# Kernel tuning notes

Hardware: AMD Instinct MI355X
Metric: run time of the kernel (lower is better)

Reference implementation:

```python
import jax, jax.numpy as jnp
import numpy as np

F0_DIM, PH_DIM, MIDI_DIM, DUR_DIM = 64, 128, 64, 64
COND = 256
TOTAL = F0_DIM + PH_DIM + MIDI_DIM + DUR_DIM  # 320
EPS = 1e-5


def setup_inputs() -> dict:
    key = jax.random.key(0)
    ks = jax.random.split(key, 16)
    B, T = 16, 4096
    inp = {
        "f0": jax.random.uniform(ks[0], (B, T), jnp.float32) * 400.0 + 80.0,
        "phone": jax.random.randint(ks[1], (B, T), 0, 100, jnp.int32),
        "duration": jax.random.uniform(ks[2], (B, T), jnp.float32),
        "midi": jax.random.randint(ks[3], (B, T), 0, 128, jnp.int32),
        # f0 encoder: Linear(1,32) -> ReLU -> Linear(32,64)
        "f0_w1": jax.random.normal(ks[4], (1, F0_DIM // 2), jnp.float32) * 0.1,
        "f0_b1": jnp.zeros((F0_DIM // 2,), jnp.float32),
        "f0_w2": jax.random.normal(ks[5], (F0_DIM // 2, F0_DIM), jnp.float32) * 0.1,
        "f0_b2": jnp.zeros((F0_DIM,), jnp.float32),
        # embeddings
        "phone_table": jax.random.normal(ks[6], (100, PH_DIM), jnp.float32),
        "midi_table": jax.random.normal(ks[7], (128, MIDI_DIM), jnp.float32),
        # duration encoder: Linear(1,32) -> ReLU -> Linear(32,64)
        "dur_w1": jax.random.normal(ks[8], (1, DUR_DIM // 2), jnp.float32) * 0.1,
        "dur_b1": jnp.zeros((DUR_DIM // 2,), jnp.float32),
        "dur_w2": jax.random.normal(ks[9], (DUR_DIM // 2, DUR_DIM), jnp.float32) * 0.1,
        "dur_b2": jnp.zeros((DUR_DIM,), jnp.float32),
        # projection: Linear(320,256) -> LayerNorm(256) -> ReLU -> Linear(256,256)
        "proj_w1": jax.random.normal(ks[10], (TOTAL, COND), jnp.float32) * (1.0 / np.sqrt(TOTAL)),
        "proj_b1": jnp.zeros((COND,), jnp.float32),
        "ln_g": jnp.ones((COND,), jnp.float32),
        "ln_b": jnp.zeros((COND,), jnp.float32),
        "proj_w2": jax.random.normal(ks[11], (COND, COND), jnp.float32) * (1.0 / np.sqrt(COND)),
        "proj_b2": jnp.zeros((COND,), jnp.float32),
    }
    return inp


def reference(f0, phone, duration, midi,
              f0_w1, f0_b1, f0_w2, f0_b2,
              phone_table, midi_table,
              dur_w1, dur_b1, dur_w2, dur_b2,
              proj_w1, proj_b1, ln_g, ln_b, proj_w2, proj_b2):
    # f0 / duration MLPs, vectorized over all (batch, time) positions
    f0_h = jax.nn.relu(f0[..., None] * f0_w1[0] + f0_b1)            # [B,T,32]
    f0_emb = f0_h @ f0_w2 + f0_b2                                    # [B,T,64]
    dur_h = jax.nn.relu(duration[..., None] * dur_w1[0] + dur_b1)    # [B,T,32]
    dur_emb = dur_h @ dur_w2 + dur_b2                                # [B,T,64]
    phone_emb = phone_table[phone]                                   # [B,T,128]
    midi_emb = midi_table[midi]                                      # [B,T,64]
    combined = jnp.concatenate([f0_emb, phone_emb, midi_emb, dur_emb], axis=-1)  # [B,T,320]
    h = combined @ proj_w1 + proj_b1                                 # [B,T,256]
    mu = jnp.mean(h, axis=-1, keepdims=True)
    var = jnp.mean((h - mu) ** 2, axis=-1, keepdims=True)
    h = (h - mu) * jax.lax.rsqrt(var + EPS) * ln_g + ln_b
    h = jax.nn.relu(h)
    return h @ proj_w2 + proj_b2                                     # [B,T,256]
```

## Files before the change

### kernel.cpp

```cpp
#include <hip/hip_runtime.h>

typedef _Float16 f16x8 __attribute__((ext_vector_type(8)));
typedef float f32x4 __attribute__((ext_vector_type(4)));
typedef unsigned int u32x2 __attribute__((ext_vector_type(2)));

#define MROWS 65536
#define BM 64
#define NBLK (MROWS / BM)

#define B1F_OFF 0u
#define B2F_OFF 65536u
#define TP_OFF 196608u
#define TM_OFF 299008u
#define BC_OFF 430080u
#define WFD_OFF 431104u


__device__ __forceinline__ unsigned afoff(unsigned X) {
  return (X * 16u) ^ ((X & 0x38u) << 1);
}

__global__ __launch_bounds__(256) void prep_tables(
    const float* __restrict__ f0_w2, const float* __restrict__ f0_b2,
    const float* __restrict__ ptab, const float* __restrict__ mtab,
    const float* __restrict__ dur_w2, const float* __restrict__ dur_b2,
    const float* __restrict__ W1, const float* __restrict__ pb1,
    float* __restrict__ wsf) {
  const int r = blockIdx.x, n = threadIdx.x;
  if (r < 64) {
    float s = 0.f;
    if (r < 32) {
      for (int j = 0; j < 64; ++j) s = fmaf(f0_w2[r * 64 + j], W1[j * 256 + n], s);
    } else {
      for (int j = 0; j < 64; ++j) s = fmaf(dur_w2[(r - 32) * 64 + j], W1[(256 + j) * 256 + n], s);
    }
    wsf[WFD_OFF / 4 + r * 256 + n] = s;
  } else if (r < 164) {
    const int p = r - 64;
    float s = 0.f;
    for (int j = 0; j < 128; ++j) s = fmaf(ptab[p * 128 + j], W1[(64 + j) * 256 + n], s);
    wsf[TP_OFF / 4 + p * 256 + n] = s;
  } else if (r < 292) {
    const int m = r - 164;
    float s = 0.f;
    for (int j = 0; j < 64; ++j) s = fmaf(mtab[m * 64 + j], W1[(192 + j) * 256 + n], s);
    wsf[TM_OFF / 4 + m * 256 + n] = s;
  } else {
    float s = pb1[n];
    for (int j = 0; j < 64; ++j) {
      s = fmaf(f0_b2[j], W1[j * 256 + n], s);
      s = fmaf(dur_b2[j], W1[(256 + j) * 256 + n], s);
    }
    wsf[BC_OFF / 4 + n] = s;
  }
}

__global__ __launch_bounds__(64) void prep_frags(const float* __restrict__ W2, char* __restrict__ ws) {
  const float* Wfd = (const float*)(ws + WFD_OFF);
  const int t = blockIdx.x;
  const int l = threadIdx.x;
  const int qq = l >> 4, c = l & 15;
  if (t < 64) {
    const int kt = t >> 4, nt = t & 15;
    const int col = (nt >> 2) * 64 + c * 4 + (nt & 3);
    f16x8 v;
#pragma unroll
    for (int e = 0; e < 8; ++e) {
      const int k = kt * 32 + 4 * qq + (e & 3) + 16 * (e >> 2);
      v[e] = (_Float16)Wfd[(k & 63) * 256 + col];
    }
    *(f16x8*)(ws + B1F_OFF + (unsigned)((kt * 16 + nt) * 64 + l) * 16u) = v;
  } else {
    const int t2 = t - 64;
    const int kt = t2 >> 4, nt = t2 & 15;
    const int col = (nt >> 2) * 64 + c * 4 + (nt & 3);
    f16x8 v;
#pragma unroll
    for (int e = 0; e < 8; ++e) {
      const int k = kt * 32 + 4 * qq + (e & 3) + 16 * (e >> 2);
      v[e] = (_Float16)W2[k * 256 + col];
    }
    *(f16x8*)(ws + B2F_OFF + (unsigned)((kt * 16 + nt) * 64 + l) * 16u) = v;
  }
}

__global__ __launch_bounds__(256, 2) void cond_enc_main(
    const float* __restrict__ f0g, const int* __restrict__ phone,
    const float* __restrict__ durg, const int* __restrict__ midi,
    const float* __restrict__ f0_w1, const float* __restrict__ f0_b1,
    const float* __restrict__ dur_w1, const float* __restrict__ dur_b1,
    const float* __restrict__ ln_g, const float* __restrict__ ln_b,
    const float* __restrict__ pb2, const char* __restrict__ ws,
    float* __restrict__ out) {
  __shared__ __align__(16) unsigned char smem[32768 + 3072];
  unsigned char* Afrag = smem;
  float* partials = (float*)(smem + 32768);

  const int tid = threadIdx.x;
  const int l = tid & 63;
  const int wc = tid >> 6;
  const int q = l >> 4;
  const int c = l & 15;
  const int b = blockIdx.x;

  const float* Tp = (const float*)(ws + TP_OFF);
  const float* Tm = (const float*)(ws + TM_OFF);

  const float xf_all = f0g[b * BM + l];
  const float xd_all = durg[b * BM + l];
  const int ph_all = phone[b * BM + l];
  const int md_all = midi[b * BM + l];

  const f32x4 zero4 = {0.f, 0.f, 0.f, 0.f};
  f32x4 acc[4][4];
#pragma unroll
  for (int i = 0; i < 4; ++i)
#pragma unroll
    for (int j = 0; j < 4; ++j) acc[i][j] = zero4;
  {
    const f16x8* B1p = (const f16x8*)(ws + B1F_OFF);
#pragma unroll
    for (int h = 0; h < 2; ++h) {
      f16x8 a1[2][4];
#pragma unroll
      for (int ii = 0; ii < 2; ++ii) {
        const int i = h * 2 + ii;
        const float xf = __shfl(xf_all, i * 16 + c);
        const float xd = __shfl(xd_all, i * 16 + c);
#pragma unroll
        for (int kh = 0; kh < 2; ++kh) {
          f16x8 hi, lo;
#pragma unroll
          for (int e = 0; e < 8; ++e) {
            const int ki = 4 * q + (e & 3) + 16 * (e >> 2);
            const float wv = kh ? dur_w1[ki] : f0_w1[ki];
            const float bv = kh ? dur_b1[ki] : f0_b1[ki];
            const float x = kh ? xd : xf;
            const float a = fmaxf(fmaf(x, wv, bv), 0.f);
            const _Float16 hh = (_Float16)a;
            hi[e] = hh;
            lo[e] = (_Float16)(a - (float)hh);
          }
          a1[ii][kh] = hi;
          a1[ii][kh + 2] = lo;
        }
      }
#pragma unroll
      for (int kt = 0; kt < 4; ++kt) {
        f16x8 b4[4];
#pragma unroll
        for (int j = 0; j < 4; ++j) b4[j] = B1p[(kt * 16 + wc * 4 + j) * 64 + l];
#pragma unroll
        for (int ii = 0; ii < 2; ++ii)
#pragma unroll
          for (int j = 0; j < 4; ++j)
            acc[h * 2 + ii][j] =
                __builtin_amdgcn_mfma_f32_16x16x32_f16(a1[ii][kt], b4[j], acc[h * 2 + ii][j], 0, 0, 0);
      }
    }
  }

  const f32x4 bc4 = *(const f32x4*)((const float*)(ws + BC_OFF) + wc * 64 + c * 4);
  float psum[4][4], psq[4][4];
#pragma unroll
  for (int i = 0; i < 4; ++i) {
#pragma unroll
    for (int r = 0; r < 4; ++r) {
      const int ph = __shfl(ph_all, i * 16 + q * 4 + r);
      const int md = __shfl(md_all, i * 16 + q * 4 + r);
      const f32x4 tp4 = *(const f32x4*)(Tp + ph * 256 + wc * 64 + c * 4);
      const f32x4 tm4 = *(const f32x4*)(Tm + md * 256 + wc * 64 + c * 4);
      float s = 0.f, ss = 0.f;
#pragma unroll
      for (int j = 0; j < 4; ++j) {
        float v = acc[i][j][r] + bc4[j] + tp4[j] + tm4[j];
        acc[i][j][r] = v;
        s += v;
        ss = fmaf(v, v, ss);
      }
      psum[i][r] = s;
      psq[i][r] = ss;
    }
  }
#pragma unroll
  for (int i = 0; i < 4; ++i)
#pragma unroll
    for (int r = 0; r < 4; ++r) {
      float s = psum[i][r], ss = psq[i][r];
#pragma unroll
      for (int m = 1; m < 16; m <<= 1) {
        s += __shfl_xor(s, m, 64);
        ss += __shfl_xor(ss, m, 64);
      }
      psum[i][r] = s;
      psq[i][r] = ss;
    }
  if (c == 0) {
#pragma unroll
    for (int i = 0; i < 4; ++i)
#pragma unroll
      for (int r = 0; r < 4; ++r) {
        const int row = i * 16 + q * 4 + r;
        partials[row * 12 + wc * 2 + 0] = psum[i][r];
        partials[row * 12 + wc * 2 + 1] = psq[i][r];
      }
  }
  __syncthreads();

  const f32x4 g4 = *(const f32x4*)(ln_g + wc * 64 + c * 4);
  const f32x4 lb4 = *(const f32x4*)(ln_b + wc * 64 + c * 4);
  const int kt_pk = wc * 2 + (c >> 3);
  const int lp_base = 16 * (c & 3);
  const unsigned hoff = (unsigned)((c >> 2) & 1) * 8u;
#pragma unroll
  for (int i = 0; i < 4; ++i) {
#pragma unroll
    for (int r = 0; r < 4; ++r) {
      const int row = i * 16 + q * 4 + r;
      const f32x4 pa = *(const f32x4*)(partials + row * 12);
      const f32x4 pb = *(const f32x4*)(partials + row * 12 + 4);
      const float s = pa[0] + pa[2] + pb[0] + pb[2];
      const float ss = pa[1] + pa[3] + pb[1] + pb[3];
      const float mu = s * (1.f / 256.f);
      const float var = fmaxf(ss * (1.f / 256.f) - mu * mu, 0.f);
      const float rstd = rsqrtf(var + 1e-5f);
      unsigned short hw[4];
#pragma unroll
      for (int j = 0; j < 4; ++j) {
        float v = fmaf((acc[i][j][r] - mu) * rstd, g4[j], lb4[j]);
        v = fmaxf(v, 0.f);
        hw[j] = __builtin_bit_cast(unsigned short, (_Float16)v);
      }
      u32x2 pkt;
      pkt[0] = (unsigned)hw[0] | ((unsigned)hw[1] << 16);
      pkt[1] = (unsigned)hw[2] | ((unsigned)hw[3] << 16);
      const unsigned X = (unsigned)((kt_pk * 4 + i) * 64 + (q * 4 + r + lp_base));
      *(u32x2*)(Afrag + afoff(X) + hoff) = pkt;
    }
  }
  __syncthreads();

#pragma unroll
  for (int i = 0; i < 4; ++i)
#pragma unroll
    for (int j = 0; j < 4; ++j) acc[i][j] = zero4;
  {
    const f16x8* B2p = (const f16x8*)(ws + B2F_OFF);
#pragma unroll
    for (int kt = 0; kt < 8; ++kt) {
      f16x8 a4[4], b4[4];
#pragma unroll
      for (int i = 0; i < 4; ++i)
        a4[i] = *(const f16x8*)(Afrag + afoff((unsigned)((kt * 4 + i) * 64 + l)));
#pragma unroll
      for (int j = 0; j < 4; ++j) b4[j] = B2p[(kt * 16 + wc * 4 + j) * 64 + l];
#pragma unroll
      for (int i = 0; i < 4; ++i)
#pragma unroll
        for (int j = 0; j < 4; ++j)
          acc[i][j] = __builtin_amdgcn_mfma_f32_16x16x32_f16(a4[i], b4[j], acc[i][j], 0, 0, 0);
    }
  }
  const f32x4 b24 = *(const f32x4*)(pb2 + wc * 64 + c * 4);
#pragma unroll
  for (int i = 0; i < 4; ++i)
#pragma unroll
    for (int r = 0; r < 4; ++r) {
      const int grow = b * BM + i * 16 + q * 4 + r;
      f32x4 st;
#pragma unroll
      for (int j = 0; j < 4; ++j) st[j] = acc[i][j][r] + b24[j];
      __builtin_nontemporal_store(st, (f32x4*)(out + grow * 256 + wc * 64 + c * 4));
    }
}

extern "C" void kernel_launch(void* const* d_in, const int* in_sizes, int n_in,
                              void* d_out, int out_size, void* d_ws, size_t ws_size,
                              hipStream_t stream) {
  (void)in_sizes; (void)n_in; (void)out_size; (void)ws_size;
  const float* f0 = (const float*)d_in[0];
  const int* phone = (const int*)d_in[1];
  const float* dur = (const float*)d_in[2];
  const int* midi = (const int*)d_in[3];
  const float* f0_w1 = (const float*)d_in[4];
  const float* f0_b1 = (const float*)d_in[5];
  const float* f0_w2 = (const float*)d_in[6];
  const float* f0_b2 = (const float*)d_in[7];
  const float* ptab = (const float*)d_in[8];
  const float* mtab = (const float*)d_in[9];
  const float* dur_w1 = (const float*)d_in[10];
  const float* dur_b1 = (const float*)d_in[11];
  const float* dur_w2 = (const float*)d_in[12];
  const float* dur_b2 = (const float*)d_in[13];
  const float* W1 = (const float*)d_in[14];
  const float* pb1 = (const float*)d_in[15];
  const float* ln_g = (const float*)d_in[16];
  const float* ln_b = (const float*)d_in[17];
  const float* W2 = (const float*)d_in[18];
  const float* pb2 = (const float*)d_in[19];
  char* ws = (char*)d_ws;
  float* out = (float*)d_out;

  prep_tables<<<293, 256, 0, stream>>>(f0_w2, f0_b2, ptab, mtab, dur_w2, dur_b2, W1, pb1, (float*)ws);
  prep_frags<<<192, 64, 0, stream>>>(W2, ws);
  cond_enc_main<<<NBLK, 256, 0, stream>>>(f0, phone, dur, midi, f0_w1, f0_b1, dur_w1, dur_b1,
                                          ln_g, ln_b, pb2, ws, out);
}
```

Baseline: 42.30 us.

## Split fused encoder into two kernels via fp16 fragment buffer; drop hi/lo split

The fused kernel is split into two kernels when the workspace is large enough. Stage 1 computes the first projection plus LayerNorm and ReLU, then writes fp16 MFMA-ready A fragments to a 32 MB workspace buffer. Stage 2 runs the second GEMM with 512-thread blocks and no LDS staging. Separately, the first GEMM's hi/lo fp16 split of the f0/duration hidden activations is removed, halving its K and MFMA count at the cost of precision. The split adds a global round trip for the intermediate but may improve occupancy and reduce LDS pressure.

```diff
diff --git a/kernel.cpp b/kernel.cpp
--- a/kernel.cpp
+++ b/kernel.cpp
@@ -5,8 +5,6 @@
 typedef unsigned int u32x2 __attribute__((ext_vector_type(2)));
 
 #define MROWS 65536
-#define BM 64
-#define NBLK (MROWS / BM)
 
 #define B1F_OFF 0u
 #define B2F_OFF 65536u
@@ -14,6 +12,8 @@
 #define TM_OFF 299008u
 #define BC_OFF 430080u
 #define WFD_OFF 431104u
+#define HFRAG_OFF 524288u
+#define WS_NEED (524288u + 33554432u)
 
 
 __device__ __forceinline__ unsigned afoff(unsigned X) {
@@ -60,18 +60,18 @@
   const int t = blockIdx.x;
   const int l = threadIdx.x;
   const int qq = l >> 4, c = l & 15;
-  if (t < 64) {
+  if (t < 32) {
     const int kt = t >> 4, nt = t & 15;
     const int col = (nt >> 2) * 64 + c * 4 + (nt & 3);
     f16x8 v;
 #pragma unroll
     for (int e = 0; e < 8; ++e) {
       const int k = kt * 32 + 4 * qq + (e & 3) + 16 * (e >> 2);
-      v[e] = (_Float16)Wfd[(k & 63) * 256 + col];
+      v[e] = (_Float16)Wfd[k * 256 + col];
     }
     *(f16x8*)(ws + B1F_OFF + (unsigned)((kt * 16 + nt) * 64 + l) * 16u) = v;
   } else {
-    const int t2 = t - 64;
+    const int t2 = t - 32;
     const int kt = t2 >> 4, nt = t2 & 15;
     const int col = (nt >> 2) * 64 + c * 4 + (nt & 3);
     f16x8 v;
@@ -84,7 +84,208 @@
   }
 }
 
-__global__ __launch_bounds__(256, 2) void cond_enc_main(
+__global__ __launch_bounds__(256, 2) void enc_stage1(
+    const float* __restrict__ f0g, const int* __restrict__ phone,
+    const float* __restrict__ durg, const int* __restrict__ midi,
+    const float* __restrict__ f0_w1, const float* __restrict__ f0_b1,
+    const float* __restrict__ dur_w1, const float* __restrict__ dur_b1,
+    const float* __restrict__ ln_g, const float* __restrict__ ln_b,
+    const char* __restrict__ ws, char* __restrict__ hfrag) {
+  __shared__ __align__(16) float partials[64 * 12];
+
+  const int tid = threadIdx.x;
+  const int l = tid & 63;
+  const int wc = tid >> 6;
+  const int q = l >> 4;
+  const int c = l & 15;
+  const int b = blockIdx.x;
+
+  const float* Tp = (const float*)(ws + TP_OFF);
+  const float* Tm = (const float*)(ws + TM_OFF);
+
+  const float xf_all = f0g[b * 64 + l];
+  const float xd_all = durg[b * 64 + l];
+  const int ph_all = phone[b * 64 + l];
+  const int md_all = midi[b * 64 + l];
+
+  f16x8 a1[4][2];
+#pragma unroll
+  for (int i = 0; i < 4; ++i) {
+    const float xf = __shfl(xf_all, i * 16 + c);
+    const float xd = __shfl(xd_all, i * 16 + c);
+#pragma unroll
+    for (int kh = 0; kh < 2; ++kh) {
+      f16x8 v;
+#pragma unroll
+      for (int e = 0; e < 8; ++e) {
+        const int ki = 4 * q + (e & 3) + 16 * (e >> 2);
+        const float wv = kh ? dur_w1[ki] : f0_w1[ki];
+        const float bv = kh ? dur_b1[ki] : f0_b1[ki];
+        const float x = kh ? xd : xf;
+        v[e] = (_Float16)fmaxf(fmaf(x, wv, bv), 0.f);
+      }
+      a1[i][kh] = v;
+    }
+  }
+
+  const f32x4 zero4 = {0.f, 0.f, 0.f, 0.f};
+  f32x4 acc[4][4];
+#pragma unroll
+  for (int i = 0; i < 4; ++i)
+#pragma unroll
+    for (int j = 0; j < 4; ++j) acc[i][j] = zero4;
+  {
+    const f16x8* B1p = (const f16x8*)(ws + B1F_OFF);
+#pragma unroll
+    for (int kt = 0; kt < 2; ++kt) {
+      f16x8 b4[4];
+#pragma unroll
+      for (int j = 0; j < 4; ++j) b4[j] = B1p[(kt * 16 + wc * 4 + j) * 64 + l];
+#pragma unroll
+      for (int i = 0; i < 4; ++i)
+#pragma unroll
+        for (int j = 0; j < 4; ++j)
+          acc[i][j] = __builtin_amdgcn_mfma_f32_16x16x32_f16(a1[i][kt], b4[j], acc[i][j], 0, 0, 0);
+    }
+  }
+
+  const f32x4 bc4 = *(const f32x4*)((const float*)(ws + BC_OFF) + wc * 64 + c * 4);
+  float psum[4][4], psq[4][4];
+#pragma unroll
+  for (int i = 0; i < 4; ++i) {
+#pragma unroll
+    for (int r = 0; r < 4; ++r) {
+      const int ph = __shfl(ph_all, i * 16 + q * 4 + r);
+      const int md = __shfl(md_all, i * 16 + q * 4 + r);
+      const f32x4 tp4 = *(const f32x4*)(Tp + ph * 256 + wc * 64 + c * 4);
+      const f32x4 tm4 = *(const f32x4*)(Tm + md * 256 + wc * 64 + c * 4);
+      float s = 0.f, ss = 0.f;
+#pragma unroll
+      for (int j = 0; j < 4; ++j) {
+        float v = acc[i][j][r] + bc4[j] + tp4[j] + tm4[j];
+        acc[i][j][r] = v;
+        s += v;
+        ss = fmaf(v, v, ss);
+      }
+      psum[i][r] = s;
+      psq[i][r] = ss;
+    }
+  }
+#pragma unroll
+  for (int i = 0; i < 4; ++i)
+#pragma unroll
+    for (int r = 0; r < 4; ++r) {
+      float s = psum[i][r], ss = psq[i][r];
+#pragma unroll
+      for (int m = 1; m < 16; m <<= 1) {
+        s += __shfl_xor(s, m, 64);
+        ss += __shfl_xor(ss, m, 64);
+      }
+      psum[i][r] = s;
+      psq[i][r] = ss;
+    }
+  if (c == 0) {
+#pragma unroll
+    for (int i = 0; i < 4; ++i)
+#pragma unroll
+      for (int r = 0; r < 4; ++r) {
+        const int row = i * 16 + q * 4 + r;
+        partials[row * 12 + wc * 2 + 0] = psum[i][r];
+        partials[row * 12 + wc * 2 + 1] = psq[i][r];
+      }
+  }
+  __syncthreads();
+
+  float mu_r, rs_r;
+  {
+    const f32x4 pa = *(const f32x4*)(partials + l * 12);
+    const f32x4 pb = *(const f32x4*)(partials + l * 12 + 4);
+    const float s = pa[0] + pa[2] + pb[0] + pb[2];
+    const float ss = pa[1] + pa[3] + pb[1] + pb[3];
+    mu_r = s * (1.f / 256.f);
+    const float var = fmaxf(ss * (1.f / 256.f) - mu_r * mu_r, 0.f);
+    rs_r = rsqrtf(var + 1e-5f);
+  }
+
+  const f32x4 g4 = *(const f32x4*)(ln_g + wc * 64 + c * 4);
+  const f32x4 lb4 = *(const f32x4*)(ln_b + wc * 64 + c * 4);
+  const int kt_pk = wc * 2 + (c >> 3);
+  const int lp_base = 16 * (c & 3);
+  const unsigned hoff = (unsigned)((c >> 2) & 1) * 8u;
+  char* hb = hfrag + (size_t)b * 32768u;
+#pragma unroll
+  for (int i = 0; i < 4; ++i) {
+#pragma unroll
+    for (int r = 0; r < 4; ++r) {
+      const int row = i * 16 + q * 4 + r;
+      const float mu = __shfl(mu_r, row, 64);
+      const float rstd = __shfl(rs_r, row, 64);
+      unsigned short hw[4];
+#pragma unroll
+      for (int j = 0; j < 4; ++j) {
+        float v = fmaf((acc[i][j][r] - mu) * rstd, g4[j], lb4[j]);
+        v = fmaxf(v, 0.f);
+        hw[j] = __builtin_bit_cast(unsigned short, (_Float16)v);
+      }
+      u32x2 pkt;
+      pkt[0] = (unsigned)hw[0] | ((unsigned)hw[1] << 16);
+      pkt[1] = (unsigned)hw[2] | ((unsigned)hw[3] << 16);
+      const unsigned g = (unsigned)((kt_pk * 4 + i) * 64 + (q * 4 + r + lp_base));
+      *(u32x2*)(hb + g * 16u + hoff) = pkt;
+    }
+  }
+}
+
+__global__ __launch_bounds__(512, 2) void enc_stage2(
+    const float* __restrict__ pb2, const char* __restrict__ ws,
+    const char* __restrict__ hfrag, float* __restrict__ out) {
+  const int tid = threadIdx.x;
+  const int l = tid & 63;
+  const int w = tid >> 6;
+  const int wc = w & 3;
+  const int wr = w >> 2;
+  const int q = l >> 4;
+  const int c = l & 15;
+  const int b2 = blockIdx.x * 2 + wr;
+
+  const f16x8* Ap = (const f16x8*)(hfrag + (size_t)b2 * 32768u);
+  const f16x8* B2p = (const f16x8*)(ws + B2F_OFF);
+
+  const f32x4 zero4 = {0.f, 0.f, 0.f, 0.f};
+  f32x4 acc[4][4];
+#pragma unroll
+  for (int i = 0; i < 4; ++i)
+#pragma unroll
+    for (int j = 0; j < 4; ++j) acc[i][j] = zero4;
+
+#pragma unroll
+  for (int kt = 0; kt < 8; ++kt) {
+    f16x8 a4[4], b4[4];
+#pragma unroll
+    for (int i = 0; i < 4; ++i) a4[i] = Ap[(kt * 4 + i) * 64 + l];
+#pragma unroll
+    for (int j = 0; j < 4; ++j) b4[j] = B2p[(kt * 16 + wc * 4 + j) * 64 + l];
+#pragma unroll
+    for (int i = 0; i < 4; ++i)
+#pragma unroll
+      for (int j = 0; j < 4; ++j)
+        acc[i][j] = __builtin_amdgcn_mfma_f32_16x16x32_f16(a4[i], b4[j], acc[i][j], 0, 0, 0);
+  }
+
+  const f32x4 b24 = *(const f32x4*)(pb2 + wc * 64 + c * 4);
+#pragma unroll
+  for (int i = 0; i < 4; ++i)
+#pragma unroll
+    for (int r = 0; r < 4; ++r) {
+      const int grow = b2 * 64 + i * 16 + q * 4 + r;
+      f32x4 st;
+#pragma unroll
+      for (int j = 0; j < 4; ++j) st[j] = acc[i][j][r] + b24[j];
+      __builtin_nontemporal_store(st, (f32x4*)(out + grow * 256 + wc * 64 + c * 4));
+    }
+}
+
+__global__ __launch_bounds__(256, 2) void cond_enc_fused(
     const float* __restrict__ f0g, const int* __restrict__ phone,
     const float* __restrict__ durg, const int* __restrict__ midi,
     const float* __restrict__ f0_w1, const float* __restrict__ f0_b1,
@@ -106,10 +307,10 @@
   const float* Tp = (const float*)(ws + TP_OFF);
   const float* Tm = (const float*)(ws + TM_OFF);
 
-  const float xf_all = f0g[b * BM + l];
-  const float xd_all = durg[b * BM + l];
-  const int ph_all = phone[b * BM + l];
-  const int md_all = midi[b * BM + l];
+  const float xf_all = f0g[b * 64 + l];
+  const float xd_all = durg[b * 64 + l];
+  const int ph_all = phone[b * 64 + l];
+  const int md_all = midi[b * 64 + l];
 
   const f32x4 zero4 = {0.f, 0.f, 0.f, 0.f};
   f32x4 acc[4][4];
@@ -120,42 +321,31 @@
   {
     const f16x8* B1p = (const f16x8*)(ws + B1F_OFF);
 #pragma unroll
-    for (int h = 0; h < 2; ++h) {
-      f16x8 a1[2][4];
-#pragma unroll
-      for (int ii = 0; ii < 2; ++ii) {
-        const int i = h * 2 + ii;
-        const float xf = __shfl(xf_all, i * 16 + c);
-        const float xd = __shfl(xd_all, i * 16 + c);
-#pragma unroll
-        for (int kh = 0; kh < 2; ++kh) {
-          f16x8 hi, lo;
-#pragma unroll
-          for (int e = 0; e < 8; ++e) {
-            const int ki = 4 * q + (e & 3) + 16 * (e >> 2);
-            const float wv = kh ? dur_w1[ki] : f0_w1[ki];
-            const float bv = kh ? dur_b1[ki] : f0_b1[ki];
-            const float x = kh ? xd : xf;
-            const float a = fmaxf(fmaf(x, wv, bv), 0.f);
-            const _Float16 hh = (_Float16)a;
-            hi[e] = hh;
-            lo[e] = (_Float16)(a - (float)hh);
-          }
-          a1[ii][kh] = hi;
-          a1[ii][kh + 2] = lo;
+    for (int i = 0; i < 4; ++i) {
+      f16x8 a1[2];
+      const float xf = __shfl(xf_all, i * 16 + c);
+      const float xd = __shfl(xd_all, i * 16 + c);
+#pragma unroll
+      for (int kh = 0; kh < 2; ++kh) {
+        f16x8 v;
+#pragma unroll
+        for (int e = 0; e < 8; ++e) {
+          const int ki = 4 * q + (e & 3) + 16 * (e >> 2);
+          const float wv = kh ? dur_w1[ki] : f0_w1[ki];
+          const float bv = kh ? dur_b1[ki] : f0_b1[ki];
+          const float x = kh ? xd : xf;
+          v[e] = (_Float16)fmaxf(fmaf(x, wv, bv), 0.f);
         }
-      }
-#pragma unroll
-      for (int kt = 0; kt < 4; ++kt) {
+        a1[kh] = v;
+      }
+#pragma unroll
+      for (int kt = 0; kt < 2; ++kt) {
         f16x8 b4[4];
 #pragma unroll
         for (int j = 0; j < 4; ++j) b4[j] = B1p[(kt * 16 + wc * 4 + j) * 64 + l];
 #pragma unroll
-        for (int ii = 0; ii < 2; ++ii)
-#pragma unroll
-          for (int j = 0; j < 4; ++j)
-            acc[h * 2 + ii][j] =
-                __builtin_amdgcn_mfma_f32_16x16x32_f16(a1[ii][kt], b4[j], acc[h * 2 + ii][j], 0, 0, 0);
+        for (int j = 0; j < 4; ++j)
+          acc[i][j] = __builtin_amdgcn_mfma_f32_16x16x32_f16(a1[kt], b4[j], acc[i][j], 0, 0, 0);
       }
     }
   }
@@ -266,7 +456,7 @@
   for (int i = 0; i < 4; ++i)
 #pragma unroll
     for (int r = 0; r < 4; ++r) {
-      const int grow = b * BM + i * 16 + q * 4 + r;
+      const int grow = b * 64 + i * 16 + q * 4 + r;
       f32x4 st;
 #pragma unroll
       for (int j = 0; j < 4; ++j) st[j] = acc[i][j][r] + b24[j];
@@ -277,7 +467,7 @@
 extern "C" void kernel_launch(void* const* d_in, const int* in_sizes, int n_in,
                               void* d_out, int out_size, void* d_ws, size_t ws_size,
                               hipStream_t stream) {
-  (void)in_sizes; (void)n_in; (void)out_size; (void)ws_size;
+  (void)in_sizes; (void)n_in; (void)out_size;
   const float* f0 = (const float*)d_in[0];
   const int* phone = (const int*)d_in[1];
   const float* dur = (const float*)d_in[2];
@@ -302,7 +492,13 @@
   float* out = (float*)d_out;
 
   prep_tables<<<293, 256, 0, stream>>>(f0_w2, f0_b2, ptab, mtab, dur_w2, dur_b2, W1, pb1, (float*)ws);
-  prep_frags<<<192, 64, 0, stream>>>(W2, ws);
-  cond_enc_main<<<NBLK, 256, 0, stream>>>(f0, phone, dur, midi, f0_w1, f0_b1, dur_w1, dur_b1,
-                                          ln_g, ln_b, pb2, ws, out);
-}
+  prep_frags<<<160, 64, 0, stream>>>(W2, ws);
+  if (ws_size >= (size_t)WS_NEED) {
+    enc_stage1<<<1024, 256, 0, stream>>>(f0, phone, dur, midi, f0_w1, f0_b1, dur_w1, dur_b1,
+                                         ln_g, ln_b, ws, ws + HFRAG_OFF);
+    enc_stage2<<<512, 512, 0, stream>>>(pb2, ws, ws + HFRAG_OFF, out);
+  } else {
+    cond_enc_fused<<<1024, 256, 0, stream>>>(f0, phone, dur, midi, f0_w1, f0_b1, dur_w1, dur_b1,
+                                             ln_g, ln_b, pb2, ws, out);
+  }
+}
```

Result: slower. 60.68 us (+43.5%).
